# Optimization experiments

Hardware: AMD Instinct MI355X
Metric: run time of the kernel (lower is better)

Reference implementation:

```python
import jax, jax.numpy as jnp
import numpy as np

B, L, T = 8, 4096, 128
D_H, D_G, D_PROJ = 1024, 256, 256


def setup_inputs() -> dict:
    key = jax.random.key(0)
    k1, k2, k3, k4, k5 = jax.random.split(key, 5)
    H = jax.random.normal(k1, (B, L, D_H), dtype=jnp.float32)
    G = jax.random.normal(k2, (B, T, D_G), dtype=jnp.float32)
    mask = jax.random.randint(k3, (B, L), 0, 2) == 1  # True = masked out
    Wk = jax.random.normal(k4, (D_H, D_PROJ), dtype=jnp.float32) * 0.02
    Wq = jax.random.normal(k5, (D_G, D_PROJ), dtype=jnp.float32) * 0.02
    return {"H": H, "G": G, "mask": mask, "Wk": Wk, "Wq": Wq}


def reference(H, G, mask, Wk, Wq):
    scale = D_PROJ ** (-0.5)
    K = jnp.einsum('bld,dp->blp', H, Wk)          # [B, L, d_proj]
    Q = jnp.einsum('btd,dp->btp', G, Wq)          # [B, T, d_proj]
    logits = jnp.einsum('btp,blp->btl', Q, K) * scale  # [B, T, L]
    logits = jnp.where(mask[:, None, :], -jnp.inf, logits)
    alpha = jax.nn.softmax(logits, axis=-1)       # [B, T, L]
    Z = jnp.einsum('btl,bld->btd', alpha, H)      # [B, T, d_h]
    return Z
```

## Files before the change

### kernel.cpp

```cpp
#include <hip/hip_runtime.h>
#include <hip/hip_bf16.h>
#include <math.h>

#define B_  8
#define L_  4096
#define T_  128
#define DH  1024
#define DG  256
#define DP  256
#define BK  64

typedef short bf16x8 __attribute__((ext_vector_type(8)));
typedef float f32x4  __attribute__((ext_vector_type(4)));

#define AS1(p) ((const __attribute__((address_space(1))) void*)(p))
#define AS3(p) ((__attribute__((address_space(3))) void*)(p))

__device__ __forceinline__ unsigned short f2bf(float f) {
    unsigned u = __float_as_uint(f);
    unsigned r = (u + 0x7FFFu + ((u >> 16) & 1u)) >> 16;
    return (unsigned short)r;
}

__global__ __launch_bounds__(256) void wct_kernel(const float* __restrict__ Wk,
                                                  const float* __restrict__ Wq,
                                                  unsigned short* __restrict__ Wct) {
    __shared__ __attribute__((aligned(16))) unsigned short As[128 * BK];
    __shared__ __attribute__((aligned(16))) unsigned short Bs[64 * BK];
    const int n0 = blockIdx.x * 64, m0 = blockIdx.y * 128;
    const int tid = threadIdx.x, wave = tid >> 6, lane = tid & 63;
    const int lm = lane & 15, quad = lane >> 4;
    const int wm = wave >> 1, wn = wave & 1;
    const int bc = (tid & 15) * 4, br = tid >> 4;
    f32x4 acc[4][2] = {};

    for (int k0 = 0; k0 < DP; k0 += BK) {
        #pragma unroll
        for (int s = 0; s < 8; ++s) {
            const int row = br + s * 16;
            const float4 v = *(const float4*)(Wk + (size_t)(m0 + row) * DP + k0 + bc);
            ushort4 p; p.x = f2bf(v.x); p.y = f2bf(v.y); p.z = f2bf(v.z); p.w = f2bf(v.w);
            *(ushort4*)(&As[row * BK + bc]) = p;
        }
        #pragma unroll
        for (int s = 0; s < 4; ++s) {
            const int row = br + s * 16;
            const float4 v = *(const float4*)(Wq + (size_t)(n0 + row) * DP + k0 + bc);
            ushort4 p; p.x = f2bf(v.x); p.y = f2bf(v.y); p.z = f2bf(v.z); p.w = f2bf(v.w);
            *(ushort4*)(&Bs[row * BK + bc]) = p;
        }
        __syncthreads();
        #pragma unroll
        for (int ks = 0; ks < 2; ++ks) {
            bf16x8 a[4], bf[2];
            #pragma unroll
            for (int i = 0; i < 4; ++i)
                a[i] = *(const bf16x8*)(&As[(wm * 64 + i * 16 + lm) * BK + ks * 32 + quad * 8]);
            #pragma unroll
            for (int j = 0; j < 2; ++j)
                bf[j] = *(const bf16x8*)(&Bs[(wn * 32 + j * 16 + lm) * BK + ks * 32 + quad * 8]);
            #pragma unroll
            for (int i = 0; i < 4; ++i)
                #pragma unroll
                for (int j = 0; j < 2; ++j)
                    acc[i][j] = __builtin_amdgcn_mfma_f32_16x16x32_bf16(a[i], bf[j], acc[i][j], 0, 0, 0);
        }
        __syncthreads();
    }
    unsigned short* Cb = Wct + (size_t)m0 * DG + n0;
    #pragma unroll
    for (int i = 0; i < 4; ++i)
        #pragma unroll
        for (int j = 0; j < 2; ++j)
            #pragma unroll
            for (int r = 0; r < 4; ++r)
                Cb[(size_t)(wm * 64 + i * 16 + quad * 4 + r) * DG + wn * 32 + j * 16 + lm] =
                    f2bf(acc[i][j][r] * 0.0625f);
}

__global__ __launch_bounds__(256) void qproj_kernel(const float* __restrict__ G,
                                                    const unsigned short* __restrict__ Wct,
                                                    unsigned short* __restrict__ Qk) {
    __shared__ __attribute__((aligned(16))) unsigned short As[128 * BK];
    __shared__ __attribute__((aligned(16))) unsigned short Bs[64 * BK];
    const int n0 = blockIdx.x * 64, m0 = blockIdx.y * 128;
    const int tid = threadIdx.x, wave = tid >> 6, lane = tid & 63;
    const int lm = lane & 15, quad = lane >> 4;
    const int wm = wave >> 1, wn = wave & 1;
    const int bc = (tid & 15) * 4, br = tid >> 4;
    const int ar = lane >> 3, akb = (lane & 7) * 8;
    f32x4 acc[4][2] = {};

    for (int k0 = 0; k0 < DG; k0 += BK) {
        #pragma unroll
        for (int s = 0; s < 8; ++s) {
            const int row = br + s * 16;
            const float4 v = *(const float4*)(G + (size_t)(m0 + row) * DG + k0 + bc);
            ushort4 p; p.x = f2bf(v.x); p.y = f2bf(v.y); p.z = f2bf(v.z); p.w = f2bf(v.w);
            *(ushort4*)(&As[row * BK + bc]) = p;
        }
        #pragma unroll
        for (int s = 0; s < 2; ++s) {
            const int rowb = s * 32 + wave * 8;
            const unsigned short* gp = Wct + (size_t)(n0 + rowb + ar) * DG + k0 + akb;
            __builtin_amdgcn_global_load_lds(AS1(gp), AS3(&Bs[rowb * BK]), 16, 0, 0);
        }
        __syncthreads();
        #pragma unroll
        for (int ks = 0; ks < 2; ++ks) {
            bf16x8 a[4], bf[2];
            #pragma unroll
            for (int i = 0; i < 4; ++i)
                a[i] = *(const bf16x8*)(&As[(wm * 64 + i * 16 + lm) * BK + ks * 32 + quad * 8]);
            #pragma unroll
            for (int j = 0; j < 2; ++j)
                bf[j] = *(const bf16x8*)(&Bs[(wn * 32 + j * 16 + lm) * BK + ks * 32 + quad * 8]);
            #pragma unroll
            for (int i = 0; i < 4; ++i)
                #pragma unroll
                for (int j = 0; j < 2; ++j)
                    acc[i][j] = __builtin_amdgcn_mfma_f32_16x16x32_bf16(a[i], bf[j], acc[i][j], 0, 0, 0);
        }
        __syncthreads();
    }
    unsigned short* Cb = Qk + (size_t)m0 * DH + n0;
    #pragma unroll
    for (int i = 0; i < 4; ++i)
        #pragma unroll
        for (int j = 0; j < 2; ++j)
            #pragma unroll
            for (int r = 0; r < 4; ++r)
                Cb[(size_t)(wm * 64 + i * 16 + quad * 4 + r) * DH + wn * 32 + j * 16 + lm] =
                    f2bf(acc[i][j][r]);
}

__global__ __launch_bounds__(256, 2) void logits_kernel(const unsigned short* __restrict__ Qk,
                                                        const float* __restrict__ H,
                                                        float* __restrict__ part) {
    __shared__ __attribute__((aligned(16))) unsigned short As[T_ * BK];
    __shared__ __attribute__((aligned(16))) unsigned short Bs[128 * BK];
    const int l0 = blockIdx.x * 128, b = blockIdx.y, h = blockIdx.z;
    const int tid = threadIdx.x, wave = tid >> 6, lane = tid & 63;
    const unsigned short* Ab = Qk + (size_t)b * T_ * DH + h * 512;
    const float*          Hb = H + ((size_t)b * L_ + l0) * DH + h * 512;

    const int lm = lane & 15, quad = lane >> 4;
    const int wm = wave >> 1, wn = wave & 1;
    f32x4 acc[4][4] = {};
    const int ar = lane >> 3, akb = (lane & 7) * 8;
    const int bc = (tid & 15) * 4, br = tid >> 4;

    for (int k0 = 0; k0 < 512; k0 += BK) {
        #pragma unroll
        for (int s = 0; s < 4; ++s) {
            const int rowb = s * 32 + wave * 8;
            const unsigned short* gp = Ab + (size_t)(rowb + ar) * DH + k0 + akb;
            __builtin_amdgcn_global_load_lds(AS1(gp), AS3(&As[rowb * BK]), 16, 0, 0);
        }
        #pragma unroll
        for (int s = 0; s < 8; ++s) {
            const int row = br + s * 16;
            const float4 v = *(const float4*)(Hb + (size_t)row * DH + k0 + bc);
            ushort4 p; p.x = f2bf(v.x); p.y = f2bf(v.y); p.z = f2bf(v.z); p.w = f2bf(v.w);
            *(ushort4*)(&Bs[row * BK + bc]) = p;
        }
        __syncthreads();
        #pragma unroll
        for (int ks = 0; ks < 2; ++ks) {
            bf16x8 a[4], bf[4];
            #pragma unroll
            for (int i = 0; i < 4; ++i)
                a[i] = *(const bf16x8*)(&As[(wm * 64 + i * 16 + lm) * BK + ks * 32 + quad * 8]);
            #pragma unroll
            for (int j = 0; j < 4; ++j)
                bf[j] = *(const bf16x8*)(&Bs[(wn * 64 + j * 16 + lm) * BK + ks * 32 + quad * 8]);
            #pragma unroll
            for (int i = 0; i < 4; ++i)
                #pragma unroll
                for (int j = 0; j < 4; ++j)
                    acc[i][j] = __builtin_amdgcn_mfma_f32_16x16x32_bf16(a[i], bf[j], acc[i][j], 0, 0, 0);
        }
        __syncthreads();
    }
    float* Cb = part + ((size_t)h * B_ + b) * T_ * L_ + l0;
    #pragma unroll
    for (int i = 0; i < 4; ++i)
        #pragma unroll
        for (int j = 0; j < 4; ++j)
            #pragma unroll
            for (int r = 0; r < 4; ++r)
                Cb[(size_t)(wm * 64 + i * 16 + quad * 4 + r) * L_ + wn * 64 + j * 16 + lm] = acc[i][j][r];
}

__global__ __launch_bounds__(256) void softmax_kernel(const float* __restrict__ part,
                                                      const int* __restrict__ mask,
                                                      unsigned short* __restrict__ alpha) {
    const int row = blockIdx.x;
    const int b   = row >> 7;
    const int tid = threadIdx.x;
    const float4* p0 = (const float4*)(part + (size_t)row * L_);
    const float4* p1 = (const float4*)(part + (size_t)B_ * T_ * L_ + (size_t)row * L_);
    const int4*   m4 = (const int4*)(mask + (size_t)b * L_);

    float vals[4][4];
    float vmax = -3.0e38f;
    #pragma unroll
    for (int s = 0; s < 4; ++s) {
        const int idx = tid + s * 256;
        const float4 a = p0[idx], c = p1[idx];
        const int4 mm = m4[idx];
        float4 v;
        v.x = mm.x ? -3.0e38f : a.x + c.x;
        v.y = mm.y ? -3.0e38f : a.y + c.y;
        v.z = mm.z ? -3.0e38f : a.z + c.z;
        v.w = mm.w ? -3.0e38f : a.w + c.w;
        vals[s][0] = v.x; vals[s][1] = v.y; vals[s][2] = v.z; vals[s][3] = v.w;
        vmax = fmaxf(vmax, fmaxf(fmaxf(v.x, v.y), fmaxf(v.z, v.w)));
    }
    #pragma unroll
    for (int off = 32; off; off >>= 1) vmax = fmaxf(vmax, __shfl_down(vmax, off, 64));

    __shared__ float red[4];
    __shared__ float bcast;
    const int wid = tid >> 6, lane = tid & 63;
    if (lane == 0) red[wid] = vmax;
    __syncthreads();
    if (tid == 0) bcast = fmaxf(fmaxf(red[0], red[1]), fmaxf(red[2], red[3]));
    __syncthreads();
    const float m = bcast;

    float sum = 0.f;
    #pragma unroll
    for (int s = 0; s < 4; ++s)
        #pragma unroll
        for (int i = 0; i < 4; ++i) {
            vals[s][i] = __expf(vals[s][i] - m);
            sum += vals[s][i];
        }
    #pragma unroll
    for (int off = 32; off; off >>= 1) sum += __shfl_down(sum, off, 64);
    __syncthreads();
    if (lane == 0) red[wid] = sum;
    __syncthreads();
    if (tid == 0) bcast = red[0] + red[1] + red[2] + red[3];
    __syncthreads();
    const float inv = 1.0f / bcast;

    unsigned short* arow = alpha + (size_t)row * L_;
    #pragma unroll
    for (int s = 0; s < 4; ++s) {
        ushort4 p;
        p.x = f2bf(vals[s][0] * inv); p.y = f2bf(vals[s][1] * inv);
        p.z = f2bf(vals[s][2] * inv); p.w = f2bf(vals[s][3] * inv);
        *(ushort4*)(arow + (size_t)(tid + s * 256) * 4) = p;
    }
}

__global__ __launch_bounds__(256, 2) void z_kernel(const unsigned short* __restrict__ alpha,
                                                   const float* __restrict__ H,
                                                   float* __restrict__ Z) {
    __shared__ __attribute__((aligned(16))) unsigned short As[T_ * BK];
    __shared__ __attribute__((aligned(16))) unsigned B32[128 * 33];
    const int d0 = blockIdx.x * 128, b = blockIdx.y, ch = blockIdx.z;
    const int tid = threadIdx.x, wave = tid >> 6, lane = tid & 63;
    const int Lc = 512;
    const unsigned short* Ab = alpha + (size_t)b * T_ * L_ + ch * Lc;
    const float*          Hb = H + ((size_t)b * L_ + ch * Lc) * DH + d0;

    const int lm = lane & 15, quad = lane >> 4;
    const int wm = wave >> 1, wn = wave & 1;
    f32x4 acc[4][4] = {};
    const int ar = lane >> 3, akb = (lane & 7) * 8;
    const int dg = tid & 15, lph = tid >> 4;

    for (int k0 = 0; k0 < Lc; k0 += BK) {
        #pragma unroll
        for (int s = 0; s < 4; ++s) {
            const int rowb = s * 32 + wave * 8;
            const unsigned short* gp = Ab + (size_t)(rowb + ar) * L_ + k0 + akb;
            __builtin_amdgcn_global_load_lds(AS1(gp), AS3(&As[rowb * BK]), 16, 0, 0);
        }
        #pragma unroll
        for (int s = 0; s < 2; ++s) {
            const int lpair = s * 16 + lph;
            const float* r0 = Hb + (size_t)(k0 + 2 * lpair) * DH + dg * 8;
            const float4 v0a = *(const float4*)(r0);
            const float4 v0b = *(const float4*)(r0 + 4);
            const float4 v1a = *(const float4*)(r0 + DH);
            const float4 v1b = *(const float4*)(r0 + DH + 4);
            float a0[8] = {v0a.x, v0a.y, v0a.z, v0a.w, v0b.x, v0b.y, v0b.z, v0b.w};
            float a1[8] = {v1a.x, v1a.y, v1a.z, v1a.w, v1b.x, v1b.y, v1b.z, v1b.w};
            #pragma unroll
            for (int i = 0; i < 8; ++i) {
                const int d = dg * 8 + i;
                B32[d * 33 + ((lpair + (d >> 3)) & 31)] =
                    (unsigned)f2bf(a0[i]) | ((unsigned)f2bf(a1[i]) << 16);
            }
        }
        __syncthreads();
        #pragma unroll
        for (int ks = 0; ks < 2; ++ks) {
            bf16x8 a[4], bf[4];
            #pragma unroll
            for (int i = 0; i < 4; ++i)
                a[i] = *(const bf16x8*)(&As[(wm * 64 + i * 16 + lm) * BK + ks * 32 + quad * 8]);
            #pragma unroll
            for (int j = 0; j < 4; ++j) {
                const int d = wn * 64 + j * 16 + lm;
                union { bf16x8 v; unsigned u[4]; } f;
                #pragma unroll
                for (int i = 0; i < 4; ++i)
                    f.u[i] = B32[d * 33 + ((ks * 16 + quad * 4 + i + (d >> 3)) & 31)];
                bf[j] = f.v;
            }
            #pragma unroll
            for (int i = 0; i < 4; ++i)
                #pragma unroll
                for (int j = 0; j < 4; ++j)
                    acc[i][j] = __builtin_amdgcn_mfma_f32_16x16x32_bf16(a[i], bf[j], acc[i][j], 0, 0, 0);
        }
        __syncthreads();
    }
    float* Cb = Z + (size_t)b * T_ * DH + d0;
    #pragma unroll
    for (int i = 0; i < 4; ++i)
        #pragma unroll
        for (int j = 0; j < 4; ++j)
            #pragma unroll
            for (int r = 0; r < 4; ++r)
                atomicAdd(&Cb[(size_t)(wm * 64 + i * 16 + quad * 4 + r) * DH + wn * 64 + j * 16 + lm],
                          acc[i][j][r]);
}

extern "C" void kernel_launch(void* const* d_in, const int* in_sizes, int n_in,
                              void* d_out, int out_size, void* d_ws, size_t ws_size,
                              hipStream_t stream) {
    const float* H    = (const float*)d_in[0];
    const float* G    = (const float*)d_in[1];
    const int*   mask = (const int*)d_in[2];
    const float* Wk   = (const float*)d_in[3];
    const float* Wq   = (const float*)d_in[4];
    float* Z = (float*)d_out;

    char* ws = (char*)d_ws;
    unsigned short* Wct   = (unsigned short*)ws;
    unsigned short* Qk    = (unsigned short*)(ws + ((size_t)1 << 20));
    float*          part  = (float*)(ws + ((size_t)4 << 20));
    unsigned short* alpha = (unsigned short*)(ws + ((size_t)40 << 20));

    hipMemsetAsync(Z, 0, (size_t)out_size * sizeof(float), stream);
    wct_kernel<<<dim3(DG / 64, DH / 128), 256, 0, stream>>>(Wk, Wq, Wct);
    qproj_kernel<<<dim3(DH / 64, (B_ * T_) / 128), 256, 0, stream>>>(G, Wct, Qk);
    logits_kernel<<<dim3(L_ / 128, B_, 2), 256, 0, stream>>>(Qk, H, part);
    softmax_kernel<<<B_ * T_, 256, 0, stream>>>(part, mask, alpha);
    z_kernel<<<dim3(DH / 128, B_, 8), 256, 0, stream>>>(alpha, H, Z);
}
```

Before: 306.1 us.

## Replace Z atomics with partial buffers plus reduce; swizzle LDS for vector loads

The z_kernel now writes per-chunk partial results to a workspace buffer, and a new reduce kernel sums them into Z. This replaces the fp32 atomicAdd epilogue and the memset of Z. The padded 33-stride LDS layout for H is replaced by a 32-stride rotated swizzle, so MFMA B fragments can be read as single 16-byte vector loads instead of four scalar reads. Each thread now loads four consecutive H rows instead of two pairs. The trade-off is an extra kernel launch and extra memory traffic for the partial buffers (8 chunks × 4 MB).

```diff
diff --git a/kernel.cpp b/kernel.cpp
--- a/kernel.cpp
+++ b/kernel.cpp
@@ -9,6 +9,8 @@
 #define DG  256
 #define DP  256
 #define BK  64
+#define ZCH 8
+#define LCH 2
 
 typedef short bf16x8 __attribute__((ext_vector_type(8)));
 typedef float f32x4  __attribute__((ext_vector_type(4)));
@@ -141,8 +143,8 @@
     __shared__ __attribute__((aligned(16))) unsigned short Bs[128 * BK];
     const int l0 = blockIdx.x * 128, b = blockIdx.y, h = blockIdx.z;
     const int tid = threadIdx.x, wave = tid >> 6, lane = tid & 63;
-    const unsigned short* Ab = Qk + (size_t)b * T_ * DH + h * 512;
-    const float*          Hb = H + ((size_t)b * L_ + l0) * DH + h * 512;
+    const unsigned short* Ab = Qk + (size_t)b * T_ * DH + h * (DH / LCH);
+    const float*          Hb = H + ((size_t)b * L_ + l0) * DH + h * (DH / LCH);
 
     const int lm = lane & 15, quad = lane >> 4;
     const int wm = wave >> 1, wn = wave & 1;
@@ -150,7 +152,7 @@
     const int ar = lane >> 3, akb = (lane & 7) * 8;
     const int bc = (tid & 15) * 4, br = tid >> 4;
 
-    for (int k0 = 0; k0 < 512; k0 += BK) {
+    for (int k0 = 0; k0 < DH / LCH; k0 += BK) {
         #pragma unroll
         for (int s = 0; s < 4; ++s) {
             const int rowb = s * 32 + wave * 8;
@@ -258,12 +260,12 @@
 
 __global__ __launch_bounds__(256, 2) void z_kernel(const unsigned short* __restrict__ alpha,
                                                    const float* __restrict__ H,
-                                                   float* __restrict__ Z) {
+                                                   float* __restrict__ part) {
     __shared__ __attribute__((aligned(16))) unsigned short As[T_ * BK];
-    __shared__ __attribute__((aligned(16))) unsigned B32[128 * 33];
+    __shared__ __attribute__((aligned(16))) unsigned B32[128 * 32];
     const int d0 = blockIdx.x * 128, b = blockIdx.y, ch = blockIdx.z;
     const int tid = threadIdx.x, wave = tid >> 6, lane = tid & 63;
-    const int Lc = 512;
+    const int Lc = L_ / ZCH;
     const unsigned short* Ab = alpha + (size_t)b * T_ * L_ + ch * Lc;
     const float*          Hb = H + ((size_t)b * L_ + ch * Lc) * DH + d0;
 
@@ -280,21 +282,25 @@
             const unsigned short* gp = Ab + (size_t)(rowb + ar) * L_ + k0 + akb;
             __builtin_amdgcn_global_load_lds(AS1(gp), AS3(&As[rowb * BK]), 16, 0, 0);
         }
-        #pragma unroll
-        for (int s = 0; s < 2; ++s) {
-            const int lpair = s * 16 + lph;
-            const float* r0 = Hb + (size_t)(k0 + 2 * lpair) * DH + dg * 8;
-            const float4 v0a = *(const float4*)(r0);
-            const float4 v0b = *(const float4*)(r0 + 4);
-            const float4 v1a = *(const float4*)(r0 + DH);
-            const float4 v1b = *(const float4*)(r0 + DH + 4);
-            float a0[8] = {v0a.x, v0a.y, v0a.z, v0a.w, v0b.x, v0b.y, v0b.z, v0b.w};
-            float a1[8] = {v1a.x, v1a.y, v1a.z, v1a.w, v1b.x, v1b.y, v1b.z, v1b.w};
+        {
+            const float* r = Hb + (size_t)(k0 + 4 * lph) * DH + dg * 8;
+            float v[4][8];
+            #pragma unroll
+            for (int rr = 0; rr < 4; ++rr) {
+                const float4 a = *(const float4*)(r + (size_t)rr * DH);
+                const float4 c = *(const float4*)(r + (size_t)rr * DH + 4);
+                v[rr][0] = a.x; v[rr][1] = a.y; v[rr][2] = a.z; v[rr][3] = a.w;
+                v[rr][4] = c.x; v[rr][5] = c.y; v[rr][6] = c.z; v[rr][7] = c.w;
+            }
+            const int lp0 = 2 * lph;
             #pragma unroll
             for (int i = 0; i < 8; ++i) {
-                const int d = dg * 8 + i;
-                B32[d * 33 + ((lpair + (d >> 3)) & 31)] =
-                    (unsigned)f2bf(a0[i]) | ((unsigned)f2bf(a1[i]) << 16);
+                const int d   = dg * 8 + i;
+                const int rot = ((i + (dg & 7)) << 2) & 31;
+                B32[d * 32 + ((lp0 + rot) & 31)] =
+                    (unsigned)f2bf(v[0][i]) | ((unsigned)f2bf(v[1][i]) << 16);
+                B32[d * 32 + ((lp0 + 1 + rot) & 31)] =
+                    (unsigned)f2bf(v[2][i]) | ((unsigned)f2bf(v[3][i]) << 16);
             }
         }
         __syncthreads();
@@ -306,12 +312,9 @@
                 a[i] = *(const bf16x8*)(&As[(wm * 64 + i * 16 + lm) * BK + ks * 32 + quad * 8]);
             #pragma unroll
             for (int j = 0; j < 4; ++j) {
-                const int d = wn * 64 + j * 16 + lm;
-                union { bf16x8 v; unsigned u[4]; } f;
-                #pragma unroll
-                for (int i = 0; i < 4; ++i)
-                    f.u[i] = B32[d * 33 + ((ks * 16 + quad * 4 + i + (d >> 3)) & 31)];
-                bf[j] = f.v;
+                const int d   = wn * 64 + j * 16 + lm;
+                const int rot = (((d & 7) + ((d >> 3) & 7)) << 2) & 31;
+                bf[j] = *(const bf16x8*)(&B32[d * 32 + ((ks * 16 + quad * 4 + rot) & 31)]);
             }
             #pragma unroll
             for (int i = 0; i < 4; ++i)
@@ -321,15 +324,27 @@
         }
         __syncthreads();
     }
-    float* Cb = Z + (size_t)b * T_ * DH + d0;
+    float* Cb = part + (((size_t)ch * B_ + b) * T_) * DH + d0;
     #pragma unroll
     for (int i = 0; i < 4; ++i)
         #pragma unroll
         for (int j = 0; j < 4; ++j)
             #pragma unroll
             for (int r = 0; r < 4; ++r)
-                atomicAdd(&Cb[(size_t)(wm * 64 + i * 16 + quad * 4 + r) * DH + wn * 64 + j * 16 + lm],
-                          acc[i][j][r]);
+                Cb[(size_t)(wm * 64 + i * 16 + quad * 4 + r) * DH + wn * 64 + j * 16 + lm] = acc[i][j][r];
+}
+
+__global__ __launch_bounds__(256) void zreduce_kernel(const float* __restrict__ p,
+                                                      float* __restrict__ Z) {
+    const size_t n = (size_t)B_ * T_ * DH;
+    const size_t i = ((size_t)blockIdx.x * 256 + threadIdx.x) * 4;
+    float4 o = {0.f, 0.f, 0.f, 0.f};
+    #pragma unroll
+    for (int c = 0; c < ZCH; ++c) {
+        const float4 a = *(const float4*)(p + (size_t)c * n + i);
+        o.x += a.x; o.y += a.y; o.z += a.z; o.w += a.w;
+    }
+    *(float4*)(Z + i) = o;
 }
 
 extern "C" void kernel_launch(void* const* d_in, const int* in_sizes, int n_in,
@@ -345,13 +360,14 @@
     char* ws = (char*)d_ws;
     unsigned short* Wct   = (unsigned short*)ws;
     unsigned short* Qk    = (unsigned short*)(ws + ((size_t)1 << 20));
-    float*          part  = (float*)(ws + ((size_t)4 << 20));
+    float*          lpart = (float*)(ws + ((size_t)4 << 20));
     unsigned short* alpha = (unsigned short*)(ws + ((size_t)40 << 20));
-
-    hipMemsetAsync(Z, 0, (size_t)out_size * sizeof(float), stream);
+    float*          zpart = (float*)(ws + ((size_t)52 << 20));
+
     wct_kernel<<<dim3(DG / 64, DH / 128), 256, 0, stream>>>(Wk, Wq, Wct);
     qproj_kernel<<<dim3(DH / 64, (B_ * T_) / 128), 256, 0, stream>>>(G, Wct, Qk);
-    logits_kernel<<<dim3(L_ / 128, B_, 2), 256, 0, stream>>>(Qk, H, part);
-    softmax_kernel<<<B_ * T_, 256, 0, stream>>>(part, mask, alpha);
-    z_kernel<<<dim3(DH / 128, B_, 8), 256, 0, stream>>>(alpha, H, Z);
-}
+    logits_kernel<<<dim3(L_ / 128, B_, LCH), 256, 0, stream>>>(Qk, H, lpart);
+    softmax_kernel<<<B_ * T_, 256, 0, stream>>>(lpart, mask, alpha);
+    z_kernel<<<dim3(DH / 128, B_, ZCH), 256, 0, stream>>>(alpha, H, zpart);
+    zreduce_kernel<<<(B_ * T_ * DH / 4) / 256, 256, 0, stream>>>(zpart, Z);
+}
```

Result: faster. 289.6 us (-5.4%).
